# Kernel tuning notes

Measured on AMD Instinct MI355X. Metric: run time of the kernel, lower is better.

The kernel has to match this reference:

```python
import jax, jax.numpy as jnp
import numpy as np


def setup_inputs() -> dict:
    key = jax.random.key(0)
    k1, k2 = jax.random.split(key)
    bs, seq_len, n_sources, input_dim = 16, 4096, 4, 257
    predictions = jax.random.normal(k1, (bs, seq_len, n_sources, input_dim), dtype=jnp.float32)
    ground_truths = jax.random.normal(k2, (bs, seq_len, n_sources, input_dim), dtype=jnp.float32)
    return {"predictions": predictions, "ground_truths": ground_truths}


def reference(predictions, ground_truths):
    # metric == 'euclidean' branch: dist[b, s] = ||pred[b,:,s,:] - gt[b,:,s,:]||_2
    diff = predictions - ground_truths                      # [bs, seq, src, dim]
    dists = jnp.sqrt(jnp.sum(diff * diff, axis=(1, 3)))     # [bs, src]
    return jnp.sum(dists)                                   # scalar loss
```

## Files before the change

kernel.cpp:

```cpp
#include <hip/hip_runtime.h>
#include <math.h>

#define BS   16
#define SEQ  4096
#define SRC  4
#define DIM  257
#define NBUCKET (BS * SRC)
#define CHUNKS 32
#define ROWS_PER_BLOCK (SEQ / CHUNKS)

__global__ __launch_bounds__(256) void bucket_sq_sums(
    const float* __restrict__ pred,
    const float* __restrict__ gt,
    float* __restrict__ ws)
{
    const int bucket = blockIdx.x;
    const int b      = bucket >> 2;
    const int src    = bucket & 3;
    const int chunk  = blockIdx.y;
    const int wave   = threadIdx.x >> 6;
    const int lane   = threadIdx.x & 63;

    const int k0    = (4 - src) & 3;
    const int n4    = (DIM - k0) >> 2;
    const int nscal = DIM - (n4 << 2);

    float acc = 0.0f;

    for (int r = wave; r < ROWS_PER_BLOCK; r += 4) {
        const int s_seq = chunk * ROWS_PER_BLOCK + r;
        const long long base =
            ((long long)(b * SEQ + s_seq) * SRC + src) * (long long)DIM;

        if (lane < n4) {
            const float4* p4 = (const float4*)(pred + base + k0);
            const float4* g4 = (const float4*)(gt   + base + k0);
            float4 p = p4[lane];
            float4 g = g4[lane];
            float dx = p.x - g.x;
            float dy = p.y - g.y;
            float dz = p.z - g.z;
            float dw = p.w - g.w;
            acc += dx * dx + dy * dy + dz * dz + dw * dw;
        }
        if (lane < nscal) {
            const int off = (lane < k0) ? lane : (k0 + (n4 << 2) + (lane - k0));
            const float d = pred[base + off] - gt[base + off];
            acc += d * d;
        }
    }

    #pragma unroll
    for (int o = 32; o > 0; o >>= 1) acc += __shfl_down(acc, o, 64);

    __shared__ float s[4];
    if (lane == 0) s[wave] = acc;
    __syncthreads();
    if (threadIdx.x == 0) {
        atomicAdd(&ws[bucket], s[0] + s[1] + s[2] + s[3]);
    }
}

__global__ void finalize_kernel(const float* __restrict__ ws,
                                float* __restrict__ out)
{
    const int t = threadIdx.x;
    float v = sqrtf(ws[t]);
    #pragma unroll
    for (int o = 32; o > 0; o >>= 1) v += __shfl_down(v, o, 64);
    if (t == 0) out[0] = v;
}

extern "C" void kernel_launch(void* const* d_in, const int* in_sizes, int n_in,
                              void* d_out, int out_size, void* d_ws, size_t ws_size,
                              hipStream_t stream)
{
    const float* pred = (const float*)d_in[0];
    const float* gt   = (const float*)d_in[1];
    float* ws  = (float*)d_ws;
    float* out = (float*)d_out;

    hipMemsetAsync(ws, 0, NBUCKET * sizeof(float), stream);

    bucket_sq_sums<<<dim3(NBUCKET, CHUNKS), 256, 0, stream>>>(pred, gt, ws);
    finalize_kernel<<<1, 64, 0, stream>>>(ws, out);
}
```

Baseline: 508.2 us.

## Stream each batch slice as flat float4 chunks with per-element source bucketing

Replaces the per-(batch,source,row) traversal, which issued misaligned row-wise loads plus scalar tails, with a flat coalesced float4 sweep over each batch slice. Each element's source index is recovered by dividing its offset by 257, and the element is added into one of four accumulators. Each block writes its partial sums to the workspace, and a two-level finalize kernel sums them, so the memset and atomics go away. This gives fully coalesced, unrolled 8-deep loads, at the cost of extra integer division and select ALU work per element.

Result: no change. 516.8 us (+1.7%).

```diff
diff --git a/kernel.cpp b/kernel.cpp
--- a/kernel.cpp
+++ b/kernel.cpp
@@ -6,69 +6,99 @@
 #define SRC  4
 #define DIM  257
 #define NBUCKET (BS * SRC)
-#define CHUNKS 32
-#define ROWS_PER_BLOCK (SEQ / CHUNKS)
+#define F4_PER_SLICE (SEQ * SRC * DIM / 4)
+#define U 8
+#define CHUNK_F4 (256 * U)
+#define NCHUNK (F4_PER_SLICE / CHUNK_F4)
+#define BLOCKS_PER_SLICE 257
 
-__global__ __launch_bounds__(256) void bucket_sq_sums(
+__global__ __launch_bounds__(256) void sq_sums(
     const float* __restrict__ pred,
     const float* __restrict__ gt,
-    float* __restrict__ ws)
+    float* __restrict__ partial)
 {
-    const int bucket = blockIdx.x;
-    const int b      = bucket >> 2;
-    const int src    = bucket & 3;
-    const int chunk  = blockIdx.y;
-    const int wave   = threadIdx.x >> 6;
-    const int lane   = threadIdx.x & 63;
+    const int b   = blockIdx.y;
+    const int blk = blockIdx.x;
+    const int t   = threadIdx.x;
 
-    const int k0    = (4 - src) & 3;
-    const int n4    = (DIM - k0) >> 2;
-    const int nscal = DIM - (n4 << 2);
+    const float4* __restrict__ p4 = (const float4*)pred;
+    const float4* __restrict__ g4 = (const float4*)gt;
+    const long long sliceBase = (long long)b * F4_PER_SLICE;
 
-    float acc = 0.0f;
+    float a0 = 0.f, a1 = 0.f, a2 = 0.f, a3 = 0.f;
 
-    for (int r = wave; r < ROWS_PER_BLOCK; r += 4) {
-        const int s_seq = chunk * ROWS_PER_BLOCK + r;
-        const long long base =
-            ((long long)(b * SEQ + s_seq) * SRC + src) * (long long)DIM;
+    for (int c = blk; c < NCHUNK; c += BLOCKS_PER_SLICE) {
+        const int f4InSlice = c * CHUNK_F4 + t;
+        const long long base = sliceBase + f4InSlice;
 
-        if (lane < n4) {
-            const float4* p4 = (const float4*)(pred + base + k0);
-            const float4* g4 = (const float4*)(gt   + base + k0);
-            float4 p = p4[lane];
-            float4 g = g4[lane];
-            float dx = p.x - g.x;
-            float dy = p.y - g.y;
-            float dz = p.z - g.z;
-            float dw = p.w - g.w;
-            acc += dx * dx + dy * dy + dz * dz + dw * dw;
-        }
-        if (lane < nscal) {
-            const int off = (lane < k0) ? lane : (k0 + (n4 << 2) + (lane - k0));
-            const float d = pred[base + off] - gt[base + off];
-            acc += d * d;
+        float4 P[U], G[U];
+        #pragma unroll
+        for (int u = 0; u < U; ++u) P[u] = p4[base + u * 256];
+        #pragma unroll
+        for (int u = 0; u < U; ++u) G[u] = g4[base + u * 256];
+
+        #pragma unroll
+        for (int u = 0; u < U; ++u) {
+            const unsigned e0 = (unsigned)(f4InSlice + u * 256) * 4u;
+            const float d0 = P[u].x - G[u].x;
+            const float d1 = P[u].y - G[u].y;
+            const float d2 = P[u].z - G[u].z;
+            const float d3 = P[u].w - G[u].w;
+            const float dd[4] = { d0*d0, d1*d1, d2*d2, d3*d3 };
+            #pragma unroll
+            for (int k = 0; k < 4; ++k) {
+                const unsigned s = ((e0 + k) / 257u) & 3u;
+                a0 += (s == 0) ? dd[k] : 0.f;
+                a1 += (s == 1) ? dd[k] : 0.f;
+                a2 += (s == 2) ? dd[k] : 0.f;
+                a3 += (s == 3) ? dd[k] : 0.f;
+            }
         }
     }
 
+    const int wave = t >> 6, lane = t & 63;
     #pragma unroll
-    for (int o = 32; o > 0; o >>= 1) acc += __shfl_down(acc, o, 64);
-
-    __shared__ float s[4];
-    if (lane == 0) s[wave] = acc;
+    for (int o = 32; o > 0; o >>= 1) {
+        a0 += __shfl_down(a0, o, 64);
+        a1 += __shfl_down(a1, o, 64);
+        a2 += __shfl_down(a2, o, 64);
+        a3 += __shfl_down(a3, o, 64);
+    }
+    __shared__ float s4[4][4];
+    if (lane == 0) { s4[wave][0]=a0; s4[wave][1]=a1; s4[wave][2]=a2; s4[wave][3]=a3; }
     __syncthreads();
-    if (threadIdx.x == 0) {
-        atomicAdd(&ws[bucket], s[0] + s[1] + s[2] + s[3]);
+    if (t < 4) {
+        const float v = s4[0][t] + s4[1][t] + s4[2][t] + s4[3][t];
+        partial[(b * 4 + t) * BLOCKS_PER_SLICE + blk] = v;
     }
 }
 
-__global__ void finalize_kernel(const float* __restrict__ ws,
-                                float* __restrict__ out)
+__global__ __launch_bounds__(256) void finalize_kernel(
+    const float* __restrict__ partial,
+    float* __restrict__ out)
 {
     const int t = threadIdx.x;
-    float v = sqrtf(ws[t]);
+    const int bucket = t >> 2;
+    const int part   = t & 3;
+    const int start  = part * 64;
+    const int cnt    = (part == 3) ? 65 : 64;
+
+    float s = 0.f;
+    for (int i = 0; i < cnt; ++i)
+        s += partial[bucket * BLOCKS_PER_SLICE + start + i];
+
+    s += __shfl_down(s, 2, 64);
+    s += __shfl_down(s, 1, 64);
+
+    float v = ((t & 3) == 0) ? sqrtf(s) : 0.f;
     #pragma unroll
     for (int o = 32; o > 0; o >>= 1) v += __shfl_down(v, o, 64);
-    if (t == 0) out[0] = v;
+
+    __shared__ float w4[4];
+    const int wave = t >> 6, lane = t & 63;
+    if (lane == 0) w4[wave] = v;
+    __syncthreads();
+    if (t == 0) out[0] = w4[0] + w4[1] + w4[2] + w4[3];
 }
 
 extern "C" void kernel_launch(void* const* d_in, const int* in_sizes, int n_in,
@@ -77,11 +107,9 @@
 {
     const float* pred = (const float*)d_in[0];
     const float* gt   = (const float*)d_in[1];
-    float* ws  = (float*)d_ws;
-    float* out = (float*)d_out;
+    float* partial = (float*)d_ws;
+    float* out     = (float*)d_out;
 
-    hipMemsetAsync(ws, 0, NBUCKET * sizeof(float), stream);
-
-    bucket_sq_sums<<<dim3(NBUCKET, CHUNKS), 256, 0, stream>>>(pred, gt, ws);
-    finalize_kernel<<<1, 64, 0, stream>>>(ws, out);
+    sq_sums<<<dim3(BLOCKS_PER_SLICE, BS), 256, 0, stream>>>(pred, gt, partial);
+    finalize_kernel<<<1, 256, 0, stream>>>(partial, out);
 }
```
